# Optimization experiments

Measured on AMD Instinct MI355X. Metric: run time of the kernel, lower is better.

## Reference

```python
import jax, jax.numpy as jnp
from jax import lax
import numpy as np

B, C, T = 512, 12, 4096
DS = 4          # int_downsize
STEPS = 7       # int_steps
KS = 51         # smooth_size
SIGMA = (KS - 1) // 2  # 25, per module: gaussian_filter1d(delta, smooth_centre)


def _gauss_kernel():
    # Replicates scipy.ndimage.gaussian_filter1d(delta, SIGMA) on a length-KS
    # delta array with default truncate=4.0 and mode='reflect'.
    r = int(4.0 * SIGMA + 0.5)
    x = np.arange(-r, r + 1)
    g = np.exp(-0.5 * (x / SIGMA) ** 2)
    g /= g.sum()
    delta = np.zeros(KS)
    delta[(KS - 1) // 2] = 1.0
    padded = np.pad(delta, r, mode='symmetric')  # scipy 'reflect' boundary
    filt = np.convolve(padded, g, mode='valid')  # len == KS (g is symmetric)
    return filt.astype(np.float32)


def resize_linear(x, factor):
    # F.interpolate(mode='linear', align_corners=False, recompute_scale_factor=False)
    Tin = x.shape[-1]
    Tout = int(Tin * factor)
    src = (jnp.arange(Tout, dtype=x.dtype) + 0.5) / factor - 0.5
    src = jnp.clip(src, 0.0, Tin - 1)
    i0 = jnp.floor(src).astype(jnp.int32)
    i1 = jnp.minimum(i0 + 1, Tin - 1)
    w = src - i0
    return x[..., i0] * (1.0 - w) + x[..., i1] * w


def resize_transform(x, factor):
    # ResizeTransformTime: resize the field AND rescale its magnitude
    if factor < 1:
        return factor * resize_linear(x, factor)
    elif factor > 1:
        return resize_linear(factor * x, factor)
    return x


def warp_1d(src, flow):
    # SpatialTransformer for 1D signals: torch fakes 2D grid_sample by repeating
    # src to [B,C,Tlen,2] and the grid to [B,1,Tlen,2]; with align_corners=True,
    # zeros padding, bilinear. The width-dim (size 2) interpolation collapses to a
    # scalar in-bounds weight xw since both width copies are identical.
    Tlen = src.shape[-1]
    new_locs = jnp.arange(Tlen, dtype=src.dtype) + flow          # [B,1,Tlen]
    v = 2.0 * (new_locs / (Tlen - 1) - 0.5)                      # normalized
    ix = (v + 1.0) * 0.5                                         # W=2 -> (W-1)=1
    iy = (v + 1.0) * 0.5 * (Tlen - 1)
    x0 = jnp.floor(ix)
    fx = ix - x0
    x0i = x0.astype(jnp.int32)
    xw = ((1.0 - fx) * ((x0i >= 0) & (x0i <= 1))
          + fx * ((x0i + 1 >= 0) & (x0i + 1 <= 1)))              # [B,1,Tlen]
    y0 = jnp.floor(iy)
    fy = iy - y0
    y0i = y0.astype(jnp.int32)
    y1i = y0i + 1
    vy0 = (y0i >= 0) & (y0i < Tlen)
    vy1 = (y1i >= 0) & (y1i < Tlen)
    y0c = jnp.clip(y0i, 0, Tlen - 1)
    y1c = jnp.clip(y1i, 0, Tlen - 1)
    Bc, Cc = src.shape[0], src.shape[1]
    idx0 = jnp.broadcast_to(y0c, (Bc, Cc, Tlen))
    idx1 = jnp.broadcast_to(y1c, (Bc, Cc, Tlen))
    g0 = jnp.take_along_axis(src, idx0, axis=-1)
    g1 = jnp.take_along_axis(src, idx1, axis=-1)
    return xw * ((1.0 - fy) * vy0 * g0 + fy * vy1 * g1)


def setup_inputs() -> dict:
    key = jax.random.key(0)
    k1, k2 = jax.random.split(key)
    source = jax.random.normal(k1, (B, C, T), dtype=jnp.float32)
    noise = jax.random.normal(k2, (B, 1, T), dtype=jnp.float32)
    flow_mag = jnp.ones((1,), dtype=jnp.float32)
    smooth_kernel = jnp.asarray(_gauss_kernel())
    return {"source": source, "flow_mag": flow_mag, "noise": noise,
            "smooth_kernel": smooth_kernel}


def reference(source, flow_mag, noise, smooth_kernel):
    flow_field = flow_mag * noise                      # [B,1,T]
    pos_flow = resize_transform(flow_field, 1.0 / DS)  # [B,1,T//DS]
    # VecInt: scaling and squaring
    vec = pos_flow * (1.0 / 2 ** STEPS)
    for _ in range(STEPS):
        vec = vec + warp_1d(vec, vec)
    pos_flow = resize_transform(vec, float(DS))        # back to [B,1,T]
    # conv1d smoothing (cross-correlation, same as F.conv1d)
    pad = (KS - 1) // 2
    pos_flow = lax.conv_general_dilated(
        pos_flow, smooth_kernel.reshape(1, 1, KS),
        window_strides=(1,), padding=[(pad, pad)],
        dimension_numbers=('NCH', 'OIH', 'NCH'))
    return warp_1d(source, pos_flow)
```

## Files before the change

kernel.cpp:

```cpp
#include <hip/hip_runtime.h>


#define BB 512
#define CC 12
#define TT 4096
#define TD 1024
#define KS 51
#define NT 1024
#define NJ 17
#define J0 (-8)
#define T_LO 32
#define T_HI 4063

typedef float f32x4 __attribute__((ext_vector_type(4)));

struct WarpW { int y0c, y1c; float w0, w1; };
struct WarpG { int addr; float a, b; };

template <int TLEN>
__device__ __forceinline__ WarpW warp_weights(int t, float flow) {
    const float tm1 = (float)(TLEN - 1);
    float nl = (float)t + flow;
    float v  = 2.0f * (nl / tm1 - 0.5f);
    float ix = (v + 1.0f) * 0.5f;
    float iy = ix * tm1;
    float x0 = floorf(ix);
    float fx = ix - x0;
    int   x0i = (int)x0;
    float m0 = (x0i >= 0 && x0i <= 1) ? 1.0f : 0.0f;
    float m1 = (x0i + 1 >= 0 && x0i + 1 <= 1) ? 1.0f : 0.0f;
    float xw = (1.0f - fx) * m0 + fx * m1;
    float y0 = floorf(iy);
    float fy = iy - y0;
    int   y0i = (int)y0;
    int   y1i = y0i + 1;
    float vy0 = (y0i >= 0 && y0i < TLEN) ? 1.0f : 0.0f;
    float vy1 = (y1i >= 0 && y1i < TLEN) ? 1.0f : 0.0f;
    WarpW r;
    r.y0c = min(max(y0i, 0), TLEN - 1);
    r.y1c = min(max(y1i, 0), TLEN - 1);
    r.w0 = xw * (1.0f - fy) * vy0;
    r.w1 = xw * fy * vy1;
    return r;
}

template <int TLEN>
__device__ __forceinline__ WarpG warp_gather(int t, float flow) {
    const float tm1 = (float)(TLEN - 1);
    float nl = (float)t + flow;
    float v  = 2.0f * (nl / tm1 - 0.5f);
    float ix = (v + 1.0f) * 0.5f;
    float iy = ix * tm1;
    float x0 = floorf(ix);
    float fx = ix - x0;
    int   x0i = (int)x0;
    float m0 = (x0i >= 0 && x0i <= 1) ? 1.0f : 0.0f;
    float m1 = (x0i + 1 >= 0 && x0i + 1 <= 1) ? 1.0f : 0.0f;
    float xw = (1.0f - fx) * m0 + fx * m1;
    float y0 = floorf(iy);
    float fy = iy - y0;
    int   y0i = (int)y0;
    int   y1i = y0i + 1;
    float vy0 = (y0i >= 0 && y0i < TLEN) ? 1.0f : 0.0f;
    float vy1 = (y1i >= 0 && y1i < TLEN) ? 1.0f : 0.0f;
    int y0c = min(max(y0i, 0), TLEN - 1);
    int y1c = min(max(y1i, 0), TLEN - 1);
    float w0 = xw * (1.0f - fy) * vy0;
    float w1 = xw * fy * vy1;
    WarpG r;
    r.addr = min(max(y0i, 0), TLEN - 2);
    int o0 = y0c - r.addr;
    int o1 = y1c - r.addr;
    r.a = (o0 ? 0.0f : w0) + (o1 ? 0.0f : w1);
    r.b = (o0 ? w0 : 0.0f) + (o1 ? w1 : 0.0f);
    return r;
}

__device__ __forceinline__ float conv_direct(const float* __restrict__ vec,
                                             const float* __restrict__ g, int t) {
    float acc = 0.0f;
    for (int k = 0; k < KS; ++k) {
        int s = t + k - 25;
        if (s < 0 || s >= TT) continue;
        float srcp = 0.25f * (float)s - 0.375f;
        srcp = fminf(fmaxf(srcp, 0.0f), (float)(TD - 1));
        float flp = floorf(srcp);
        int i0 = (int)flp;
        int i1 = min(i0 + 1, TD - 1);
        float w = srcp - flp;
        acc += g[k] * 4.0f * ((1.0f - w) * vec[i0] + w * vec[i1]);
    }
    return acc;
}

extern "C" __global__ void __launch_bounds__(NT)
rand_warp_aug_kernel(const float* __restrict__ source,
                     const float* __restrict__ flow_mag,
                     const float* __restrict__ noise,
                     const float* __restrict__ gk,
                     float* __restrict__ out) {
    __shared__ float vecA[TD];
    __shared__ float vecB[TD];
    __shared__ float buf[TT];
    __shared__ float g[KS];
    __shared__ float wtab[NJ][4];

    const int b   = blockIdx.x;
    const int tid = threadIdx.x;
    const float fm = flow_mag[0];

    const f32x4* nrow4 = (const f32x4*)(noise + (size_t)b * TT);
    {
        f32x4 nv = nrow4[tid];
        float x1 = fm * nv.y;
        float x2 = fm * nv.z;
        vecA[tid] = (x1 * 0.5f + x2 * 0.5f) * (0.25f * 0.0078125f);
    }
    if (tid < KS) g[tid] = gk[tid];
    __syncthreads();

    if (tid < 4 * NJ) {
        int p = tid / NJ;
        int j = tid % NJ + J0;
        float acc = 0.0f;
        for (int k = 0; k < KS; ++k) {
            int q = p + k - 25;
            int d = (q >= 0) ? (q >> 2) : -((-q + 3) >> 2);
            int r = q - 4 * d;
            float c = 0.0f;
            if (r == 0)      { if (j == d - 1) c = 0.375f; else if (j == d) c = 0.625f; }
            else if (r == 1) { if (j == d - 1) c = 0.125f; else if (j == d) c = 0.875f; }
            else if (r == 2) { if (j == d)     c = 0.875f; else if (j == d + 1) c = 0.125f; }
            else             { if (j == d)     c = 0.625f; else if (j == d + 1) c = 0.375f; }
            acc += g[k] * c;
        }
        wtab[tid % NJ][p] = 4.0f * acc;
    }

    float* cur = vecA;
    float* nxt = vecB;
#pragma unroll 1
    for (int s = 0; s < 7; ++s) {
        {
            float fl = cur[tid];
            WarpW w = warp_weights<TD>(tid, fl);
            nxt[tid] = fl + (w.w0 * cur[w.y0c] + w.w1 * cur[w.y1c]);
        }
        __syncthreads();
        float* tmp = cur; cur = nxt; nxt = tmp;
    }

    const int p  = tid & 3;
    const int Tb = tid >> 2;
    float pf[4];
    {
        float a0 = 0.0f, a1 = 0.0f, a2 = 0.0f, a3 = 0.0f;
#pragma unroll
        for (int j = 0; j < NJ; ++j) {
            float wreg = wtab[j][p];
            int base = Tb + j + J0;
            a0 += wreg * cur[base];
            a1 += wreg * cur[base + 256];
            a2 += wreg * cur[base + 512];
            a3 += wreg * cur[base + 768];
        }
        pf[0] = a0; pf[1] = a1; pf[2] = a2; pf[3] = a3;
    }
    if (tid < T_LO)                  pf[0] = conv_direct(cur, g, tid);
    if (tid >= NT - (TT - 1 - T_HI)) pf[3] = conv_direct(cur, g, tid + 3 * NT);

    WarpG wg[4];
#pragma unroll
    for (int tt = 0; tt < 4; ++tt)
        wg[tt] = warp_gather<TT>(tid + tt * NT, pf[tt]);

    const f32x4* sbase4 = (const f32x4*)(source + (size_t)b * CC * TT);
    float*       obase  = out + (size_t)b * CC * TT;
    f32x4 r = sbase4[tid];
#pragma unroll 1
    for (int c = 0; c < CC; ++c) {
        __syncthreads();
        ((f32x4*)buf)[tid] = r;
        if (c + 1 < CC) r = sbase4[(size_t)(c + 1) * (TT / 4) + tid];
        __syncthreads();
        float* orow = obase + (size_t)c * TT;
#pragma unroll
        for (int tt = 0; tt < 4; ++tt) {
            int t = tid + tt * NT;
            float v0 = buf[wg[tt].addr];
            float v1 = buf[wg[tt].addr + 1];
            __builtin_nontemporal_store(wg[tt].a * v0 + wg[tt].b * v1, orow + t);
        }
    }
}

extern "C" void kernel_launch(void* const* d_in, const int* in_sizes, int n_in,
                              void* d_out, int out_size, void* d_ws, size_t ws_size,
                              hipStream_t stream) {
    const float* source   = (const float*)d_in[0];
    const float* flow_mag = (const float*)d_in[1];
    const float* noise    = (const float*)d_in[2];
    const float* gk       = (const float*)d_in[3];
    float* out = (float*)d_out;

    rand_warp_aug_kernel<<<BB, NT, 0, stream>>>(source, flow_mag, noise, gk, out);
}
```

Before: 58.31 us.

## Gather warp source directly from global memory instead of LDS staging per channel

The per-channel staging of source rows through a 16KB shared buffer, with two barriers per channel, is removed. Each thread now computes its gather weights and issues 12 unaligned 2-float global loads, one per channel, before writing outputs with ordinary stores instead of nontemporal ones. The launch bound also adds a minimum-occupancy hint. This drops LDS traffic and barriers, but the global loads become gathers that rely on cache locality, and the output stores lose the nontemporal hint.

```diff
diff --git a/kernel.cpp b/kernel.cpp
--- a/kernel.cpp
+++ b/kernel.cpp
@@ -13,6 +13,7 @@
 #define T_HI 4063
 
 typedef float f32x4 __attribute__((ext_vector_type(4)));
+typedef float f32x2 __attribute__((ext_vector_type(2), aligned(4)));
 
 struct WarpW { int y0c, y1c; float w0, w1; };
 struct WarpG { int addr; float a, b; };
@@ -93,7 +94,7 @@
     return acc;
 }
 
-extern "C" __global__ void __launch_bounds__(NT)
+extern "C" __global__ void __launch_bounds__(NT, 8)
 rand_warp_aug_kernel(const float* __restrict__ source,
                      const float* __restrict__ flow_mag,
                      const float* __restrict__ noise,
@@ -101,7 +102,6 @@
                      float* __restrict__ out) {
     __shared__ float vecA[TD];
     __shared__ float vecB[TD];
-    __shared__ float buf[TT];
     __shared__ float g[KS];
     __shared__ float wtab[NJ][4];
 
@@ -169,28 +169,19 @@
     if (tid < T_LO)                  pf[0] = conv_direct(cur, g, tid);
     if (tid >= NT - (TT - 1 - T_HI)) pf[3] = conv_direct(cur, g, tid + 3 * NT);
 
-    WarpG wg[4];
+    const float* sbase = source + (size_t)b * CC * TT;
+    float*       obase = out    + (size_t)b * CC * TT;
 #pragma unroll
-    for (int tt = 0; tt < 4; ++tt)
-        wg[tt] = warp_gather<TT>(tid + tt * NT, pf[tt]);
-
-    const f32x4* sbase4 = (const f32x4*)(source + (size_t)b * CC * TT);
-    float*       obase  = out + (size_t)b * CC * TT;
-    f32x4 r = sbase4[tid];
-#pragma unroll 1
-    for (int c = 0; c < CC; ++c) {
-        __syncthreads();
-        ((f32x4*)buf)[tid] = r;
-        if (c + 1 < CC) r = sbase4[(size_t)(c + 1) * (TT / 4) + tid];
-        __syncthreads();
-        float* orow = obase + (size_t)c * TT;
+    for (int tt = 0; tt < TT / NT; ++tt) {
+        int t = tid + tt * NT;
+        WarpG w = warp_gather<TT>(t, pf[tt]);
+        f32x2 v[CC];
 #pragma unroll
-        for (int tt = 0; tt < 4; ++tt) {
-            int t = tid + tt * NT;
-            float v0 = buf[wg[tt].addr];
-            float v1 = buf[wg[tt].addr + 1];
-            __builtin_nontemporal_store(wg[tt].a * v0 + wg[tt].b * v1, orow + t);
-        }
+        for (int c = 0; c < CC; ++c)
+            v[c] = *(const f32x2*)(sbase + (size_t)c * TT + w.addr);
+#pragma unroll
+        for (int c = 0; c < CC; ++c)
+            obase[(size_t)c * TT + t] = w.a * v[c].x + w.b * v[c].y;
     }
 }
 
```

New measurement: 69.29 us. +18.8%, slower.
